# Performance work log

Hardware: AMD Instinct MI355X
Metric: run time of the kernel (lower is better)

## Reference

```python
import jax, jax.numpy as jnp
import numpy as np

R2_WEIGHT = 0.1
EVO_WEIGHT = 10.0
EVO_LAMBDA = 2.0
EPS = 1e-8
JS_EPS = 1e-7
GROUP_SIZE = 4


def setup_inputs() -> dict:
    key = jax.random.key(0)
    k1, k2, k3, k4 = jax.random.split(key, 4)
    B, L, C = 32, 4096, 4
    logits = jax.random.normal(k1, (B, L, C), dtype=jnp.float32)
    prob = jax.random.uniform(k2, (B, L, C), dtype=jnp.float32)
    y_true = jax.random.normal(k3, (B, L, C + 1), dtype=jnp.float32)  # argmax -> label in [0, C]
    y_evo_mat = jax.random.uniform(k4, (B, B), dtype=jnp.float32)
    return {"logits": logits, "prob": prob, "y_true": y_true, "y_evo_mat": y_evo_mat}


def reference(logits, prob, y_true, y_evo_mat):
    B, L, C = prob.shape
    Cf = y_true.shape[-1]
    lbl = jnp.argmax(y_true, axis=-1)           # (B, L), value C means missing
    nonmiss = lbl != C                          # (B, L)

    # ---- cross entropy, ignore_index=C, sum / valid_count ----
    logp = jax.nn.log_softmax(logits, axis=-1)  # (B, L, C)
    safe_lbl = jnp.where(nonmiss, lbl, 0)
    nll = -jnp.take_along_axis(logp, safe_lbl[..., None], axis=-1)[..., 0]
    ce_sum = jnp.sum(jnp.where(nonmiss, nll, 0.0))
    valid = jnp.sum(nonmiss)
    ce_loss = jnp.where(valid > 0, ce_sum / jnp.maximum(valid, 1).astype(ce_sum.dtype), ce_sum)

    # ---- minimac R2 loss over groups of 4 (fully vectorized over groups) ----
    G = B // GROUP_SIZE
    ytg = y_true[: G * GROUP_SIZE].reshape(G, GROUP_SIZE, L, Cf)
    pg = prob[: G * GROUP_SIZE].reshape(G, GROUP_SIZE, L, C)
    nm = jnp.argmax(ytg, axis=-1) != C          # (G, 4, L)
    nm_cnt = nm.sum(axis=1).astype(jnp.float32)  # (G, L)
    alt_cnt = ytg[..., 1:C].sum(axis=(1, 3))     # (G, L)
    af = alt_cnt / jnp.maximum(nm_cnt, 1.0)      # (G, L)
    pred_alt = pg[..., 1:C].sum(axis=-1).mean(axis=1)  # (G, L)
    miss = ~nm                                   # (G, 4, L) -- broadcasts like torch code
    taf = jnp.where(miss, 0.5, af[:, None, :])   # (G, 4, L)
    edge = (taf == 0.0) | (taf == 1.0)
    denom = jnp.maximum(taf * (1.0 - taf), 0.01)
    r2 = jnp.square(pred_alt[:, None, :] - taf) / denom
    r2 = jnp.where(edge | miss, 0.0, r2)
    group_r2 = -r2                               # (G, 4, L)
    gvm = ((nm.sum(axis=1) > 0)[:, None, :]) & (group_r2 != 0.0)
    r2_sum = group_r2.sum()
    tv = gvm.sum()
    r2_loss = R2_WEIGHT * jnp.where(tv > 0, r2_sum / jnp.maximum(tv, 1).astype(r2_sum.dtype), r2_sum)

    # ---- evo loss: batched pairwise JS divergence ----
    p = jnp.maximum(prob, JS_EPS)                # (B, L, C)
    plogp = jnp.sum(p * jnp.log(p), axis=-1)     # (B, L)
    m = 0.5 * (p[:, None] + p[None, :])          # (B, B, L, C)
    mlogm = jnp.sum(m * jnp.log(m), axis=-1)     # (B, B, L)
    # 0.5*(kl_pm + kl_qm) = 0.5*(plogp_i + plogp_j) - (m*log m).sum
    js = 0.5 * (plogp[:, None] + plogp[None, :]) - mlogm  # (B, B, L)
    same_gt = lbl[:, None] == lbl[None, :]       # (B, B, L)
    mask = nonmiss[:, None] & nonmiss[None, :] & same_gt
    js_mat = jnp.sum(jnp.where(mask, js, 0.0), axis=-1)   # (B, B)
    w = jnp.exp(-EVO_LAMBDA * y_evo_mat)
    w = w / (w.sum(axis=1, keepdims=True) + EPS)
    evo = EVO_WEIGHT * (jnp.sum(w * js_mat) / B)
    evo_loss = jnp.where(jnp.isfinite(evo), evo, 0.0)

    total_loss = 1000.0 * (ce_loss + r2_loss + evo_loss)
    return total_loss
```

## Files before the change

### kernel.cpp

```cpp
#include <hip/hip_runtime.h>
#include <math.h>

#define B 32
#define C 4
#define CF 5
#define WPB 16
#define NTHR (WPB * 64)

__global__ __launch_bounds__(NTHR) void k_main(const float* __restrict__ logits,
                                               const float* __restrict__ prob,
                                               const float* __restrict__ y_true,
                                               const float* __restrict__ yevo,
                                               float* __restrict__ partials,
                                               int L) {
    const int t = threadIdx.x;
    const int lane = t & 63;
    const int g = lane >> 5;
    const int b = lane & 31;
    const int wv = t >> 6;
    const int l = (blockIdx.x << 4) | wv;

    __shared__ float w[1024];
    __shared__ float wred[WPB][5];

    {
        float e = __expf(-2.0f * yevo[t]);
        float s = e;
        s += __shfl_xor(s, 1);
        s += __shfl_xor(s, 2);
        s += __shfl_xor(s, 4);
        s += __shfl_xor(s, 8);
        s += __shfl_xor(s, 16);
        w[t] = e / (s + 1e-8f);
    }

    float ce = 0.f, valid = 0.f, r2s = 0.f, tv = 0.f;

    const float* yt = y_true + ((size_t)b * L + l) * CF;
    float y0 = yt[0], y1 = yt[1], y2 = yt[2], y3 = yt[3], y4 = yt[4];
    int lbl = 0; float best = y0;
    if (y1 > best) { best = y1; lbl = 1; }
    if (y2 > best) { best = y2; lbl = 2; }
    if (y3 > best) { best = y3; lbl = 3; }
    if (y4 > best) { best = y4; lbl = 4; }
    float salt = y1 + y2 + y3;

    float4 pv = *(const float4*)(prob + ((size_t)b * L + l) * C);
    float spalt = pv.y + pv.z + pv.w;
    float q0 = fmaxf(pv.x, 1e-7f), q1 = fmaxf(pv.y, 1e-7f);
    float q2 = fmaxf(pv.z, 1e-7f), q3 = fmaxf(pv.w, 1e-7f);
    float plp = q0 * __logf(q0) + q1 * __logf(q1)
              + q2 * __logf(q2) + q3 * __logf(q3);

    if (g == 0) {
        if (lbl != 4) {
            float4 av = *(const float4*)(logits + ((size_t)b * L + l) * C);
            float mx = fmaxf(fmaxf(av.x, av.y), fmaxf(av.z, av.w));
            float se = __expf(av.x - mx) + __expf(av.y - mx)
                     + __expf(av.z - mx) + __expf(av.w - mx);
            float lse = mx + __logf(se);
            float al = (lbl == 0) ? av.x : (lbl == 1) ? av.y
                     : (lbl == 2) ? av.z : av.w;
            ce = lse - al;
            valid = 1.f;
        }
        float nmc = (lbl != 4) ? 1.f : 0.f, altc = salt, ps = spalt;
        nmc  += __shfl_xor(nmc, 1);   nmc  += __shfl_xor(nmc, 2);
        altc += __shfl_xor(altc, 1);  altc += __shfl_xor(altc, 2);
        ps   += __shfl_xor(ps, 1);    ps   += __shfl_xor(ps, 2);
        float af = altc / fmaxf(nmc, 1.f);
        float pred = 0.25f * ps;
        bool miss = (lbl == 4);
        float taf = miss ? 0.5f : af;
        bool edge = (taf == 0.f) || (taf == 1.f);
        float denom = fmaxf(taf * (1.f - taf), 0.01f);
        float d = pred - taf;
        float r2 = d * d / denom;
        if (edge || miss) r2 = 0.f;
        r2s -= r2;
        if (nmc > 0.f && r2 != 0.f) tv += 1.f;
    }

    __syncthreads();

    float evo = 0.f;
    #pragma unroll
    for (int it = 0; it < 8; ++it) {
        int d = 1 + it + (g << 3);
        int jj = (b + d) & 31;
        int src = (lane & 32) | jj;
        float qj0 = __shfl(q0, src), qj1 = __shfl(q1, src);
        float qj2 = __shfl(q2, src), qj3 = __shfl(q3, src);
        float pj  = __shfl(plp, src);
        int   lj  = __shfl(lbl, src);
        float m0 = 0.5f * (q0 + qj0), m1 = 0.5f * (q1 + qj1);
        float m2 = 0.5f * (q2 + qj2), m3 = 0.5f * (q3 + qj3);
        float mlogm = m0 * __logf(m0) + m1 * __logf(m1)
                    + m2 * __logf(m2) + m3 * __logf(m3);
        float js = 0.5f * (plp + pj) - mlogm;
        bool act = (lbl == lj) && (lbl != 4) && !((d == 16) & (b >= 16));
        float wf = act ? (w[(b << 5) + jj] + w[(jj << 5) + b]) : 0.f;
        evo = fmaf(wf, js, evo);
    }

    #pragma unroll
    for (int off = 32; off; off >>= 1) {
        ce += __shfl_xor(ce, off);   valid += __shfl_xor(valid, off);
        r2s += __shfl_xor(r2s, off); tv += __shfl_xor(tv, off);
        evo += __shfl_xor(evo, off);
    }
    if (lane == 0) {
        wred[wv][0] = ce; wred[wv][1] = valid; wred[wv][2] = r2s;
        wred[wv][3] = tv; wred[wv][4] = evo;
    }
    __syncthreads();

    if (t < 16) {
        float a0 = wred[t][0], a1 = wred[t][1], a2 = wred[t][2],
              a3 = wred[t][3], a4 = wred[t][4];
        a0 += __shfl_xor(a0, 1); a1 += __shfl_xor(a1, 1);
        a2 += __shfl_xor(a2, 1); a3 += __shfl_xor(a3, 1);
        a4 += __shfl_xor(a4, 1);
        a0 += __shfl_xor(a0, 2); a1 += __shfl_xor(a1, 2);
        a2 += __shfl_xor(a2, 2); a3 += __shfl_xor(a3, 2);
        a4 += __shfl_xor(a4, 2);
        a0 += __shfl_xor(a0, 4); a1 += __shfl_xor(a1, 4);
        a2 += __shfl_xor(a2, 4); a3 += __shfl_xor(a3, 4);
        a4 += __shfl_xor(a4, 4);
        a0 += __shfl_xor(a0, 8); a1 += __shfl_xor(a1, 8);
        a2 += __shfl_xor(a2, 8); a3 += __shfl_xor(a3, 8);
        a4 += __shfl_xor(a4, 8);
        if (t == 0) {
            float* p = partials + (size_t)blockIdx.x * 8;
            p[0] = a0; p[1] = a1; p[2] = a2; p[3] = a3; p[4] = a4;
        }
    }
}

__global__ __launch_bounds__(256) void k_final(const float* __restrict__ partials,
                                               float* __restrict__ out, int nblk) {
    __shared__ float wred[4][5];
    const int t = threadIdx.x;
    float s0 = 0.f, s1 = 0.f, s2 = 0.f, s3 = 0.f, s4 = 0.f;
    if (t < nblk) {
        const float* p = partials + (size_t)t * 8;
        s0 = p[0]; s1 = p[1]; s2 = p[2]; s3 = p[3]; s4 = p[4];
    }
    #pragma unroll
    for (int off = 32; off; off >>= 1) {
        s0 += __shfl_xor(s0, off); s1 += __shfl_xor(s1, off);
        s2 += __shfl_xor(s2, off); s3 += __shfl_xor(s3, off);
        s4 += __shfl_xor(s4, off);
    }
    const int wv = t >> 6;
    if ((t & 63) == 0) {
        wred[wv][0] = s0; wred[wv][1] = s1; wred[wv][2] = s2;
        wred[wv][3] = s3; wred[wv][4] = s4;
    }
    __syncthreads();
    if (t == 0) {
        float ce_sum = wred[0][0] + wred[1][0] + wred[2][0] + wred[3][0];
        float vcnt   = wred[0][1] + wred[1][1] + wred[2][1] + wred[3][1];
        float r2_sum = wred[0][2] + wred[1][2] + wred[2][2] + wred[3][2];
        float tvs    = wred[0][3] + wred[1][3] + wred[2][3] + wred[3][3];
        float evo_s  = wred[0][4] + wred[1][4] + wred[2][4] + wred[3][4];
        float ce_loss = (vcnt > 0.f) ? (ce_sum / fmaxf(vcnt, 1.f)) : ce_sum;
        float r2_loss = 0.1f * ((tvs > 0.f) ? (r2_sum / fmaxf(tvs, 1.f)) : r2_sum);
        float evo = 10.f * (evo_s / 32.f);
        if (!isfinite(evo)) evo = 0.f;
        out[0] = 1000.f * (ce_loss + r2_loss + evo);
    }
}

extern "C" void kernel_launch(void* const* d_in, const int* in_sizes, int n_in,
                              void* d_out, int out_size, void* d_ws, size_t ws_size,
                              hipStream_t stream) {
    const float* logits = (const float*)d_in[0];
    const float* prob   = (const float*)d_in[1];
    const float* y_true = (const float*)d_in[2];
    const float* yevo   = (const float*)d_in[3];
    float* out = (float*)d_out;

    const int L = in_sizes[0] / (B * C);
    const int nblk = L / WPB;

    float* partials = (float*)d_ws;

    k_main<<<nblk, NTHR, 0, stream>>>(logits, prob, y_true, yevo, partials, L);
    k_final<<<1, 256, 0, stream>>>(partials, out, nblk);
}
```

Before: 15.33 us.

## Load per-position data once with coalesced mapping and stage through shared memory

Before, each wave loaded y_true and prob twice, once per half-wave, with a stride of L across batch rows. Now the first 512 threads each load one (b,l) element, with 16 consecutive l per b so accesses are more contiguous, and stage q/plp/lbl into shared memory. The other 512 threads compute the evo weight matrix at the same time. Partials are stored structure-of-arrays, and the final kernel loops over them, which also handles nblk>256. The cost is extra shared memory and an LDS round trip per block.

```diff
diff --git a/kernel.cpp b/kernel.cpp
--- a/kernel.cpp
+++ b/kernel.cpp
@@ -12,49 +12,44 @@
                                                const float* __restrict__ y_true,
                                                const float* __restrict__ yevo,
                                                float* __restrict__ partials,
-                                               int L) {
+                                               int L, int nblk) {
     const int t = threadIdx.x;
-    const int lane = t & 63;
-    const int g = lane >> 5;
-    const int b = lane & 31;
-    const int wv = t >> 6;
-    const int l = (blockIdx.x << 4) | wv;
+    const int blk = blockIdx.x;
+    const int l0 = blk << 4;
 
     __shared__ float w[1024];
+    __shared__ float sq0[WPB][33], sq1[WPB][33], sq2[WPB][33], sq3[WPB][33];
+    __shared__ float sm[WPB][33];
+    __shared__ int   sl[WPB][33];
     __shared__ float wred[WPB][5];
 
-    {
-        float e = __expf(-2.0f * yevo[t]);
-        float s = e;
-        s += __shfl_xor(s, 1);
-        s += __shfl_xor(s, 2);
-        s += __shfl_xor(s, 4);
-        s += __shfl_xor(s, 8);
-        s += __shfl_xor(s, 16);
-        w[t] = e / (s + 1e-8f);
-    }
-
     float ce = 0.f, valid = 0.f, r2s = 0.f, tv = 0.f;
 
-    const float* yt = y_true + ((size_t)b * L + l) * CF;
-    float y0 = yt[0], y1 = yt[1], y2 = yt[2], y3 = yt[3], y4 = yt[4];
-    int lbl = 0; float best = y0;
-    if (y1 > best) { best = y1; lbl = 1; }
-    if (y2 > best) { best = y2; lbl = 2; }
-    if (y3 > best) { best = y3; lbl = 3; }
-    if (y4 > best) { best = y4; lbl = 4; }
-    float salt = y1 + y2 + y3;
-
-    float4 pv = *(const float4*)(prob + ((size_t)b * L + l) * C);
-    float spalt = pv.y + pv.z + pv.w;
-    float q0 = fmaxf(pv.x, 1e-7f), q1 = fmaxf(pv.y, 1e-7f);
-    float q2 = fmaxf(pv.z, 1e-7f), q3 = fmaxf(pv.w, 1e-7f);
-    float plp = q0 * __logf(q0) + q1 * __logf(q1)
-              + q2 * __logf(q2) + q3 * __logf(q3);
-
-    if (g == 0) {
+    if (t < 512) {
+        const int b = t >> 4, ll = t & 15;
+        const int l = l0 + ll;
+        const float* yt = y_true + ((size_t)b * L + l) * CF;
+        float y0 = yt[0], y1 = yt[1], y2 = yt[2], y3 = yt[3], y4 = yt[4];
+        float4 pv = *(const float4*)(prob + ((size_t)b * L + l) * C);
+        float4 av = *(const float4*)(logits + ((size_t)b * L + l) * C);
+
+        int lbl = 0; float best = y0;
+        if (y1 > best) { best = y1; lbl = 1; }
+        if (y2 > best) { best = y2; lbl = 2; }
+        if (y3 > best) { best = y3; lbl = 3; }
+        if (y4 > best) { best = y4; lbl = 4; }
+        float salt = y1 + y2 + y3;
+
+        float spalt = pv.y + pv.z + pv.w;
+        float q0 = fmaxf(pv.x, 1e-7f), q1 = fmaxf(pv.y, 1e-7f);
+        float q2 = fmaxf(pv.z, 1e-7f), q3 = fmaxf(pv.w, 1e-7f);
+        float plp = q0 * __logf(q0) + q1 * __logf(q1)
+                  + q2 * __logf(q2) + q3 * __logf(q3);
+
+        sq0[ll][b] = q0; sq1[ll][b] = q1; sq2[ll][b] = q2; sq3[ll][b] = q3;
+        sm[ll][b] = plp; sl[ll][b] = lbl;
+
         if (lbl != 4) {
-            float4 av = *(const float4*)(logits + ((size_t)b * L + l) * C);
             float mx = fmaxf(fmaxf(av.x, av.y), fmaxf(av.z, av.w));
             float se = __expf(av.x - mx) + __expf(av.y - mx)
                      + __expf(av.z - mx) + __expf(av.w - mx);
@@ -64,10 +59,11 @@
             ce = lse - al;
             valid = 1.f;
         }
+
         float nmc = (lbl != 4) ? 1.f : 0.f, altc = salt, ps = spalt;
-        nmc  += __shfl_xor(nmc, 1);   nmc  += __shfl_xor(nmc, 2);
-        altc += __shfl_xor(altc, 1);  altc += __shfl_xor(altc, 2);
-        ps   += __shfl_xor(ps, 1);    ps   += __shfl_xor(ps, 2);
+        nmc  += __shfl_xor(nmc, 16);  nmc  += __shfl_xor(nmc, 32);
+        altc += __shfl_xor(altc, 16); altc += __shfl_xor(altc, 32);
+        ps   += __shfl_xor(ps, 16);   ps   += __shfl_xor(ps, 32);
         float af = altc / fmaxf(nmc, 1.f);
         float pred = 0.25f * ps;
         bool miss = (lbl == 4);
@@ -79,9 +75,30 @@
         if (edge || miss) r2 = 0.f;
         r2s -= r2;
         if (nmc > 0.f && r2 != 0.f) tv += 1.f;
-    }
-
+    } else {
+        int t2 = t - 512;
+        int i = t2 >> 4, jh = t2 & 15;
+        float2 ye = *(const float2*)(yevo + i * 32 + 2 * jh);
+        float e0 = __expf(-2.f * ye.x), e1 = __expf(-2.f * ye.y);
+        float s = e0 + e1;
+        s += __shfl_xor(s, 1);
+        s += __shfl_xor(s, 2);
+        s += __shfl_xor(s, 4);
+        s += __shfl_xor(s, 8);
+        float inv = 1.f / (s + 1e-8f);
+        w[i * 32 + 2 * jh]     = e0 * inv;
+        w[i * 32 + 2 * jh + 1] = e1 * inv;
+    }
     __syncthreads();
+
+    const int lane = t & 63;
+    const int g = lane >> 5;
+    const int b = lane & 31;
+    const int wv = t >> 6;
+
+    float q0 = sq0[wv][b], q1 = sq1[wv][b], q2 = sq2[wv][b], q3 = sq3[wv][b];
+    float plp = sm[wv][b];
+    int   lbl = sl[wv][b];
 
     float evo = 0.f;
     #pragma unroll
@@ -118,21 +135,18 @@
     if (t < 16) {
         float a0 = wred[t][0], a1 = wred[t][1], a2 = wred[t][2],
               a3 = wred[t][3], a4 = wred[t][4];
-        a0 += __shfl_xor(a0, 1); a1 += __shfl_xor(a1, 1);
-        a2 += __shfl_xor(a2, 1); a3 += __shfl_xor(a3, 1);
-        a4 += __shfl_xor(a4, 1);
-        a0 += __shfl_xor(a0, 2); a1 += __shfl_xor(a1, 2);
-        a2 += __shfl_xor(a2, 2); a3 += __shfl_xor(a3, 2);
-        a4 += __shfl_xor(a4, 2);
-        a0 += __shfl_xor(a0, 4); a1 += __shfl_xor(a1, 4);
-        a2 += __shfl_xor(a2, 4); a3 += __shfl_xor(a3, 4);
-        a4 += __shfl_xor(a4, 4);
-        a0 += __shfl_xor(a0, 8); a1 += __shfl_xor(a1, 8);
-        a2 += __shfl_xor(a2, 8); a3 += __shfl_xor(a3, 8);
-        a4 += __shfl_xor(a4, 8);
+        #pragma unroll
+        for (int off = 8; off; off >>= 1) {
+            a0 += __shfl_xor(a0, off); a1 += __shfl_xor(a1, off);
+            a2 += __shfl_xor(a2, off); a3 += __shfl_xor(a3, off);
+            a4 += __shfl_xor(a4, off);
+        }
         if (t == 0) {
-            float* p = partials + (size_t)blockIdx.x * 8;
-            p[0] = a0; p[1] = a1; p[2] = a2; p[3] = a3; p[4] = a4;
+            partials[0 * nblk + blk] = a0;
+            partials[1 * nblk + blk] = a1;
+            partials[2 * nblk + blk] = a2;
+            partials[3 * nblk + blk] = a3;
+            partials[4 * nblk + blk] = a4;
         }
     }
 }
@@ -142,9 +156,12 @@
     __shared__ float wred[4][5];
     const int t = threadIdx.x;
     float s0 = 0.f, s1 = 0.f, s2 = 0.f, s3 = 0.f, s4 = 0.f;
-    if (t < nblk) {
-        const float* p = partials + (size_t)t * 8;
-        s0 = p[0]; s1 = p[1]; s2 = p[2]; s3 = p[3]; s4 = p[4];
+    for (int idx = t; idx < nblk; idx += 256) {
+        s0 += partials[0 * nblk + idx];
+        s1 += partials[1 * nblk + idx];
+        s2 += partials[2 * nblk + idx];
+        s3 += partials[3 * nblk + idx];
+        s4 += partials[4 * nblk + idx];
     }
     #pragma unroll
     for (int off = 32; off; off >>= 1) {
@@ -186,6 +203,7 @@
 
     float* partials = (float*)d_ws;
 
-    k_main<<<nblk, NTHR, 0, stream>>>(logits, prob, y_true, yevo, partials, L);
+    k_main<<<nblk, NTHR, 0, stream>>>(logits, prob, y_true, yevo,
+                                      partials, L, nblk);
     k_final<<<1, 256, 0, stream>>>(partials, out, nblk);
 }
```

Measured after the change: 14.70 us. 4.1% less time.
